# Performance work log

Measured on AMD Instinct MI355X. Metric: run time of the kernel, lower is better.

## Reference

```python
import jax, jax.numpy as jnp
import numpy as np

B, L, F_DIM, H = 4, 384, 640, 128
K_COULOMB = 332.0
DIELECTRIC = 80.0
BN_EPS = 1e-5

# amino-acid charge table, index order 'ACDEFGHIKLMNPQRSTVWY'
_AA = 'ACDEFGHIKLMNPQRSTVWY'
_CHG = {'D': -1.0, 'E': -1.0, 'K': 1.0, 'R': 1.0, 'H': 0.1}
_TABLE = np.zeros((20, 3), dtype=np.float32)
for _i, _aa in enumerate(_AA):
    c = _CHG.get(_aa, 0.0)
    _TABLE[_i, 0 if c > 0 else (1 if c < 0 else 2)] = 1.0
CHG_TABLE = jnp.asarray(_TABLE)


def _conv1d(x, w, b, pad):
    # x: [N, Cin, L], w: [Cout, Cin, K]
    y = jax.lax.conv_general_dilated(x, w, (1,), [(pad, pad)],
                                     dimension_numbers=('NCH', 'OIH', 'NCH'))
    return y + b[None, :, None]


def setup_inputs() -> dict:
    key = jax.random.key(0)
    ks = jax.random.split(key, 32)
    s = 0.05

    def rn(k, shape):
        return (jax.random.normal(k, shape) * s).astype(jnp.float32)

    inp = {
        'features': jax.random.normal(ks[0], (B, L, F_DIM), dtype=jnp.float32),
        'seq_ids': jax.random.randint(ks[1], (B, L), 0, 20, dtype=jnp.int32),
        'structures': (jax.random.normal(ks[2], (B, L, 3)) * 10.0).astype(jnp.float32),
        # charge predictor: Linear(F,H) -> ReLU -> BN(H) -> Linear(H,H//2) -> ReLU -> Linear(H//2,3) -> Softmax
        'W1': rn(ks[3], (F_DIM, H)), 'b1': jnp.zeros((H,), jnp.float32),
        'gamma': jnp.ones((H,), jnp.float32), 'beta': jnp.zeros((H,), jnp.float32),
        'rmean': jnp.zeros((H,), jnp.float32), 'rvar': jnp.ones((H,), jnp.float32),
        'W2': rn(ks[4], (H, H // 2)), 'b2': jnp.zeros((H // 2,), jnp.float32),
        'W3': rn(ks[5], (H // 2, 3)), 'b3': jnp.zeros((3,), jnp.float32),
        # salt bridge detector: Linear(2F+1,H) -> ReLU -> Linear(H,64) -> ReLU -> Linear(64,1) -> Sigmoid
        'sW1': rn(ks[6], (2 * F_DIM + 1, H)), 'sb1': jnp.zeros((H,), jnp.float32),
        'sW2': rn(ks[7], (H, 64)), 'sb2': jnp.zeros((64,), jnp.float32),
        'sW3': rn(ks[8], (64, 1)), 'sb3': jnp.zeros((1,), jnp.float32),
        # potential calculator convs (OIH layout)
        'c1w': rn(ks[9], (16, 1, 5)), 'c1b': jnp.zeros((16,), jnp.float32),
        'c2w': rn(ks[10], (8, 16, 3)), 'c2b': jnp.zeros((8,), jnp.float32),
        'c3w': rn(ks[11], (1, 8, 3)), 'c3b': jnp.zeros((1,), jnp.float32),
    }
    return inp


def reference(features, seq_ids, structures,
              W1, b1, gamma, beta, rmean, rvar, W2, b2, W3, b3,
              sW1, sb1, sW2, sb2, sW3, sb3,
              c1w, c1b, c2w, c2b, c3w, c3b):
    b_, l_, f_ = features.shape

    # true charges from sequence (one-hot pos/neg/neutral)
    true_charges = CHG_TABLE[seq_ids]                               # [B,L,3]

    # --- charge predictor (BatchNorm in eval mode: running stats) ---
    x = features.reshape(-1, f_)
    h = jax.nn.relu(x @ W1 + b1)
    h = gamma * (h - rmean) / jnp.sqrt(rvar + BN_EPS) + beta
    h = jax.nn.relu(h @ W2 + b2)
    pc = jax.nn.softmax(h @ W3 + b3, axis=-1).reshape(b_, l_, 3)    # [B,L,3]

    net_charge = pc[:, :, 0:1] - pc[:, :, 1:2]                      # [B,L,1]

    # --- electrostatic potential: 1D conv stack on [B,1,L] ---
    p = net_charge.transpose(0, 2, 1)                               # [B,1,L]
    p = jax.nn.relu(_conv1d(p, c1w, c1b, 2))
    p = jax.nn.relu(_conv1d(p, c2w, c2b, 1))
    p = _conv1d(p, c3w, c3b, 1)
    potential = p.transpose(0, 2, 1)                                # [B,L,1]

    # --- pairwise distances ---
    diff = structures[:, :, None, :] - structures[:, None, :, :]    # [B,L,L,3]
    D = jnp.sqrt(jnp.sum(diff * diff, axis=-1) + 1e-12)             # [B,L,L]

    # --- salt bridges: vectorized edge-MLP over all (pos i, neg j) pairs ---
    pos = pc[:, :, 0] > pc[:, :, 2]                                 # [B,L]
    neg = pc[:, :, 1] > pc[:, :, 2]                                 # [B,L]
    a, bb, d = sW1[:f_], sW1[f_:2 * f_], sW1[2 * f_]                # split cat([fi,fj,dist]) @ sW1
    fi = features @ a                                               # [B,L,H]
    fj = features @ bb                                              # [B,L,H]
    hid = jax.nn.relu(fi[:, :, None, :] + fj[:, None, :, :] + D[..., None] * d + sb1)  # [B,L,L,H]
    hid2 = jax.nn.relu(hid @ sW2 + sb2)                             # [B,L,L,64]
    prob = jax.nn.sigmoid((hid2 @ sW3 + sb3)[..., 0])               # [B,L,L]
    q = pos[:, :, None] & neg[:, None, :] & (D < 4.0) & (prob > 0.5)
    salt_bridge_masks = (q | q.transpose(0, 2, 1)).astype(jnp.float32)  # [B,L,L]

    # --- Coulomb energy with distance-dependent dielectric ---
    # dielectric = eps * D / 4 -> e_ij = k * q_i q_j / (eps/4 * D^2)
    qc = pc[:, :, 0] - pc[:, :, 1]                                  # [B,L]
    valid = (D < 15.0) & (D > 0.0)
    triu = jnp.triu(jnp.ones((l_, l_), bool), k=1)[None]
    D_safe = jnp.where(valid, D, 1.0)
    e_ij = K_COULOMB * qc[:, :, None] * qc[:, None, :] / ((DIELECTRIC / 4.0) * D_safe * D_safe)
    energy = jnp.sum(jnp.where(valid & triu, e_ij, 0.0), axis=(1, 2))  # [B]

    return (pc, true_charges, net_charge, potential, salt_bridge_masks, energy)
```

## Files before the change

### kernel.cpp

```cpp
#include <hip/hip_runtime.h>

#define LSEQ 384
#define NROWS 1536
#define FDIM 640
#define HDIM 128
#define PART 196608

#define WS_H1P 0
#define WS_FIP (4*PART)
#define WS_FJP (8*PART)
#define WS_FI  (12*PART)
#define WS_FJ  (13*PART)
#define WS_QC  (14*PART)
#define WS_FLAG (WS_QC + NROWS)

#define OUT_PC    0
#define OUT_TC    4608
#define OUT_NET   9216
#define OUT_POT   10752
#define OUT_MASK  12288
#define OUT_EN    602112

__global__ __launch_bounds__(256) void k_gemm(const float* __restrict__ X,
                                              const float* __restrict__ W1,
                                              const float* __restrict__ sW1,
                                              float* __restrict__ ws,
                                              float* __restrict__ out) {
    __shared__ float As[2 * 32 * 34];
    __shared__ float Bs[2 * 32 * 64];
    const int t = threadIdx.x;
    if (blockIdx.x == 0 && blockIdx.y == 0 && blockIdx.z == 0 && t < 4)
        out[OUT_EN + t] = 0.0f;

    const int m0 = blockIdx.x * 32;
    const int gy = blockIdx.y, kz = blockIdx.z;
    const int mat = gy >> 1, half = gy & 1, n0 = half * 64;
    const float* W = (mat == 0) ? W1 : (mat == 1 ? sW1 : sW1 + 640 * 128);
    float* O = ws + (mat == 0 ? WS_H1P : (mat == 1 ? WS_FIP : WS_FJP)) + kz * PART;

    const int a_r = t >> 3, a_c = (t & 7) * 4;
    const int b_r = t >> 4, b_c = (t & 15) * 4;
    const int tx = (t & 15) * 4, ty = (t >> 4) * 2;
    const int k0 = kz * 160;

    float acc[2][4] = {};

    float4 av  = *(const float4*)&X[(m0 + a_r) * FDIM + k0 + a_c];
    float4 bv0 = *(const float4*)&W[(k0 + b_r) * HDIM + n0 + b_c];
    float4 bv1 = *(const float4*)&W[(k0 + b_r + 16) * HDIM + n0 + b_c];
    As[(a_c + 0) * 34 + a_r] = av.x;
    As[(a_c + 1) * 34 + a_r] = av.y;
    As[(a_c + 2) * 34 + a_r] = av.z;
    As[(a_c + 3) * 34 + a_r] = av.w;
    *(float4*)&Bs[b_r * 64 + b_c]        = bv0;
    *(float4*)&Bs[(b_r + 16) * 64 + b_c] = bv1;
    __syncthreads();

    for (int it = 0; it < 5; it++) {
        const int buf = it & 1;
        if (it < 4) {
            const int kk = k0 + (it + 1) * 32;
            av  = *(const float4*)&X[(m0 + a_r) * FDIM + kk + a_c];
            bv0 = *(const float4*)&W[(kk + b_r) * HDIM + n0 + b_c];
            bv1 = *(const float4*)&W[(kk + b_r + 16) * HDIM + n0 + b_c];
        }
        const float* Ab = As + buf * 1088;
        const float* Bb = Bs + buf * 2048;
#pragma unroll
        for (int k = 0; k < 32; k++) {
            float2 a = *(const float2*)&Ab[k * 34 + ty];
            float4 b = *(const float4*)&Bb[k * 64 + tx];
            acc[0][0] = fmaf(a.x, b.x, acc[0][0]);
            acc[0][1] = fmaf(a.x, b.y, acc[0][1]);
            acc[0][2] = fmaf(a.x, b.z, acc[0][2]);
            acc[0][3] = fmaf(a.x, b.w, acc[0][3]);
            acc[1][0] = fmaf(a.y, b.x, acc[1][0]);
            acc[1][1] = fmaf(a.y, b.y, acc[1][1]);
            acc[1][2] = fmaf(a.y, b.z, acc[1][2]);
            acc[1][3] = fmaf(a.y, b.w, acc[1][3]);
        }
        if (it < 4) {
            float* Aw = As + (buf ^ 1) * 1088;
            float* Bw = Bs + (buf ^ 1) * 2048;
            Aw[(a_c + 0) * 34 + a_r] = av.x;
            Aw[(a_c + 1) * 34 + a_r] = av.y;
            Aw[(a_c + 2) * 34 + a_r] = av.z;
            Aw[(a_c + 3) * 34 + a_r] = av.w;
            *(float4*)&Bw[b_r * 64 + b_c]        = bv0;
            *(float4*)&Bw[(b_r + 16) * 64 + b_c] = bv1;
            __syncthreads();
        }
    }
#pragma unroll
    for (int r = 0; r < 2; r++) {
        float4 v = make_float4(acc[r][0], acc[r][1], acc[r][2], acc[r][3]);
        *(float4*)&O[(m0 + ty + r) * HDIM + n0 + tx] = v;
    }
}

__global__ __launch_bounds__(256) void k_row(float* __restrict__ ws,
                                             const float* __restrict__ b1,
                                             const float* __restrict__ gam,
                                             const float* __restrict__ bet,
                                             const float* __restrict__ rmean,
                                             const float* __restrict__ rvar,
                                             const float* __restrict__ W2,
                                             const float* __restrict__ b2,
                                             const float* __restrict__ W3,
                                             const float* __restrict__ b3,
                                             const int* __restrict__ seq,
                                             float* __restrict__ out) {
    const int t = threadIdx.x, w = t >> 6, lane = t & 63;
    const int row = blockIdx.x * 4 + w;
    const long base = (long)row * 128;
    const float* h1p = ws + WS_H1P;
    const float* fip = ws + WS_FIP;
    const float* fjp = ws + WS_FJP;

    {
        float fi0 = fip[base + lane] + fip[PART + base + lane]
                  + fip[2 * PART + base + lane] + fip[3 * PART + base + lane];
        float fi1 = fip[base + 64 + lane] + fip[PART + base + 64 + lane]
                  + fip[2 * PART + base + 64 + lane] + fip[3 * PART + base + 64 + lane];
        float fj0 = fjp[base + lane] + fjp[PART + base + lane]
                  + fjp[2 * PART + base + lane] + fjp[3 * PART + base + lane];
        float fj1 = fjp[base + 64 + lane] + fjp[PART + base + 64 + lane]
                  + fjp[2 * PART + base + 64 + lane] + fjp[3 * PART + base + 64 + lane];
        ws[WS_FI + base + lane]      = fi0;
        ws[WS_FI + base + 64 + lane] = fi1;
        ws[WS_FJ + base + lane]      = fj0;
        ws[WS_FJ + base + 64 + lane] = fj1;
    }

    float h0 = h1p[base + lane] + h1p[PART + base + lane]
             + h1p[2 * PART + base + lane] + h1p[3 * PART + base + lane];
    float h1 = h1p[base + 64 + lane] + h1p[PART + base + 64 + lane]
             + h1p[2 * PART + base + 64 + lane] + h1p[3 * PART + base + 64 + lane];
    h0 = fmaxf(h0 + b1[lane], 0.0f);
    h1 = fmaxf(h1 + b1[64 + lane], 0.0f);
    h0 = gam[lane]      * (h0 - rmean[lane])      / sqrtf(rvar[lane] + 1e-5f)      + bet[lane];
    h1 = gam[64 + lane] * (h1 - rmean[64 + lane]) / sqrtf(rvar[64 + lane] + 1e-5f) + bet[64 + lane];

    float acc = b2[lane];
#pragma unroll
    for (int cc = 0; cc < 64; cc++) {
        float wv0 = W2[cc * 64 + lane];
        float wv1 = W2[(cc + 64) * 64 + lane];
        float hv0 = __uint_as_float(__builtin_amdgcn_readlane(__float_as_uint(h0), cc));
        float hv1 = __uint_as_float(__builtin_amdgcn_readlane(__float_as_uint(h1), cc));
        acc = fmaf(hv0, wv0, acc);
        acc = fmaf(hv1, wv1, acc);
    }
    float h2 = fmaxf(acc, 0.0f);
    float x0 = h2 * W3[lane * 3 + 0];
    float x1 = h2 * W3[lane * 3 + 1];
    float x2 = h2 * W3[lane * 3 + 2];
#pragma unroll
    for (int o = 32; o > 0; o >>= 1) {
        x0 += __shfl_xor(x0, o, 64);
        x1 += __shfl_xor(x1, o, 64);
        x2 += __shfl_xor(x2, o, 64);
    }
    if (lane == 0) {
        float l0 = x0 + b3[0], l1 = x1 + b3[1], l2 = x2 + b3[2];
        float m = fmaxf(l0, fmaxf(l1, l2));
        float e0 = expf(l0 - m), e1 = expf(l1 - m), e2 = expf(l2 - m);
        float s = e0 + e1 + e2;
        float pc0 = e0 / s, pc1 = e1 / s, pc2 = e2 / s;
        out[OUT_PC + row * 3 + 0] = pc0;
        out[OUT_PC + row * 3 + 1] = pc1;
        out[OUT_PC + row * 3 + 2] = pc2;
        float net = pc0 - pc1;
        out[OUT_NET + row] = net;
        ws[WS_QC + row] = net;
        ((int*)(ws + WS_FLAG))[row] = (pc0 > pc2 ? 1 : 0) | (pc1 > pc2 ? 2 : 0);
        int sid = seq[row];
        float c0 = (sid == 6 || sid == 8 || sid == 14) ? 1.0f : 0.0f;
        float c1 = (sid == 2 || sid == 3) ? 1.0f : 0.0f;
        out[OUT_TC + row * 3 + 0] = c0;
        out[OUT_TC + row * 3 + 1] = c1;
        out[OUT_TC + row * 3 + 2] = (c0 == 0.0f && c1 == 0.0f) ? 1.0f : 0.0f;
    }
}

__device__ __forceinline__ float mlp_eval(const float* __restrict__ fi, const float* __restrict__ fj,
                                          int gi, int gj, float D,
                                          float dv0, float dv1, float sb0, float sb1v,
                                          float b2v, float w3l, const float* __restrict__ sW2, int lane) {
    float h0 = fmaxf(fi[(long)gi * 128 + lane]      + fj[(long)gj * 128 + lane]      + D * dv0 + sb0,  0.0f);
    float h1 = fmaxf(fi[(long)gi * 128 + 64 + lane] + fj[(long)gj * 128 + 64 + lane] + D * dv1 + sb1v, 0.0f);
    float a0 = 0.0f, a1 = 0.0f;
#pragma unroll 8
    for (int cc = 0; cc < 64; cc++) {
        float hv0 = __uint_as_float(__builtin_amdgcn_readlane(__float_as_uint(h0), cc));
        float hv1 = __uint_as_float(__builtin_amdgcn_readlane(__float_as_uint(h1), cc));
        a0 = fmaf(hv0, sW2[cc * 64 + lane], a0);
        a1 = fmaf(hv1, sW2[(cc + 64) * 64 + lane], a1);
    }
    float x = fmaxf(a0 + a1 + b2v, 0.0f) * w3l;
#pragma unroll
    for (int o = 32; o > 0; o >>= 1) x += __shfl_xor(x, o, 64);
    return x;
}

__global__ __launch_bounds__(256) void k2(const float* __restrict__ S,
                                          const float* __restrict__ ws,
                                          const float* __restrict__ sW1,
                                          const float* __restrict__ sb1,
                                          const float* __restrict__ sW2,
                                          const float* __restrict__ sb2,
                                          const float* __restrict__ sW3,
                                          const float* __restrict__ sb3,
                                          const float* __restrict__ c1w, const float* __restrict__ c1b,
                                          const float* __restrict__ c2w, const float* __restrict__ c2b,
                                          const float* __restrict__ c3w, const float* __restrict__ c3b,
                                          float* __restrict__ out) {
    __shared__ char smem[6592];
    const int t = threadIdx.x;
    const int bi = blockIdx.x;

    if (bi < 4) {
        float* p0h = (float*)smem;
        const int b = bi;
        for (int idx = t; idx < 392; idx += 256)
            p0h[idx] = (idx >= 4 && idx < 388) ? out[OUT_NET + b * LSEQ + (idx - 4)] : 0.0f;
        __syncthreads();
        for (int pos = t; pos < LSEQ; pos += 256) {
            float p2v[8][3];
#pragma unroll
            for (int o2 = 0; o2 < 8; o2++) {
                float cb = c2b[o2];
#pragma unroll
                for (int d1 = 0; d1 < 3; d1++) p2v[o2][d1] = cb;
            }
            for (int i = 0; i < 16; i++) {
                float p1v[5];
#pragma unroll
                for (int d2 = 0; d2 < 5; d2++) {
                    int q2 = pos - 2 + d2;
                    float a = c1b[i];
#pragma unroll
                    for (int k = 0; k < 5; k++)
                        a = fmaf(p0h[q2 + 2 + k], c1w[i * 5 + k], a);
                    p1v[d2] = (q2 >= 0 && q2 < LSEQ) ? fmaxf(a, 0.0f) : 0.0f;
                }
#pragma unroll
                for (int o2 = 0; o2 < 8; o2++) {
#pragma unroll
                    for (int d1 = 0; d1 < 3; d1++) {
#pragma unroll
                        for (int k = 0; k < 3; k++)
                            p2v[o2][d1] = fmaf(p1v[d1 + k], c2w[(o2 * 16 + i) * 3 + k], p2v[o2][d1]);
                    }
                }
            }
            float acc3 = c3b[0];
#pragma unroll
            for (int o2 = 0; o2 < 8; o2++) {
#pragma unroll
                for (int k = 0; k < 3; k++) {
                    int q1 = pos - 1 + k;
                    float pv = (q1 >= 0 && q1 < LSEQ) ? fmaxf(p2v[o2][k], 0.0f) : 0.0f;
                    acc3 = fmaf(pv, c3w[o2 * 3 + k], acc3);
                }
            }
            out[OUT_POT + b * LSEQ + pos] = acc3;
        }
        return;
    }

    float* sx = (float*)smem;
    float* sy = sx + 384;
    float* sz = sy + 384;
    float* sq = sz + 384;
    unsigned char* sf = (unsigned char*)(sq + 384);
    float* red = (float*)(smem + 6544);

    red = (float*)(smem + 6528);

    const float* qc = ws + WS_QC;
    const int* flags = (const int*)(ws + WS_FLAG);
    const float* fi = ws + WS_FI;
    const float* fj = ws + WS_FJ;

    const int pb = bi - 4;
    const int b = pb / 96;
    const int i0 = (pb % 96) * 4;

    for (int j = t; j < LSEQ; j += 256) {
        int g = b * LSEQ + j;
        sx[j] = S[g * 3 + 0];
        sy[j] = S[g * 3 + 1];
        sz[j] = S[g * 3 + 2];
        sq[j] = qc[g];
        sf[j] = (unsigned char)flags[g];
    }
    __syncthreads();

    const int w = t >> 6, lane = t & 63;
    const int i = i0 + w;
    const int row = b * LSEQ + i;
    const float six = sx[i], siy = sy[i], siz = sz[i], qi = sq[i];
    const int fli = sf[i];
    const bool posi = (fli & 1) != 0, negi = (fli & 2) != 0;
    float* mrow = out + OUT_MASK + (long)row * LSEQ;

    const float* dvec = sW1 + 1280 * 128;
    const float dv0 = dvec[lane], dv1 = dvec[lane + 64];
    const float sb0 = sb1[lane], sb1v = sb1[lane + 64];
    const float w3l = sW3[lane];
    const float b2v = sb2[lane];
    const float b3v = sb3[0];

    float esum = 0.0f;
    for (int j0 = 0; j0 < LSEQ; j0 += 64) {
        const int j = j0 + lane;
        float dx = __fsub_rn(six, sx[j]);
        float dy = __fsub_rn(siy, sy[j]);
        float dz = __fsub_rn(siz, sz[j]);
        float d2 = __fadd_rn(__fadd_rn(__fmul_rn(dx, dx), __fmul_rn(dy, dy)), __fmul_rn(dz, dz));
        d2 = __fadd_rn(d2, 1e-12f);
        float D = __fsqrt_rn(d2);
        if (j > i && D < 15.0f && D > 0.0f) {
            float num = __fmul_rn(__fmul_rn(332.0f, qi), sq[j]);
            float den = __fmul_rn(__fmul_rn(20.0f, D), D);
            esum += __fdiv_rn(num, den);
        }
        int flj = sf[j];
        bool near = (D < 4.0f);
        bool need1 = near && posi && ((flj & 2) != 0);
        bool need2 = near && negi && ((flj & 1) != 0);
        int pk = (need1 ? 1 : 0) | (need2 ? 2 : 0);
        unsigned long long mb = __ballot(pk != 0);
        unsigned long long hitbits = 0ull;
        while (mb) {
            int jl = __ffsll((long long)mb) - 1;
            mb &= mb - 1ull;
            int pf = __shfl(pk, jl, 64);
            float Dj = __shfl(D, jl, 64);
            int gj = b * LSEQ + j0 + jl;
            bool hit = false;
            if (pf & 1) {
                float x = mlp_eval(fi, fj, row, gj, Dj, dv0, dv1, sb0, sb1v, b2v, w3l, sW2, lane);
                hit = (x + b3v) > 0.0f;
            }
            if (!hit && (pf & 2)) {
                float x = mlp_eval(fi, fj, gj, row, Dj, dv0, dv1, sb0, sb1v, b2v, w3l, sW2, lane);
                hit = (x + b3v) > 0.0f;
            }
            if (hit) hitbits |= (1ull << jl);
        }
        mrow[j] = ((hitbits >> lane) & 1ull) ? 1.0f : 0.0f;
    }
#pragma unroll
    for (int o = 32; o > 0; o >>= 1) esum += __shfl_xor(esum, o, 64);
    if (lane == 0) red[w] = esum;
    __syncthreads();
    if (t == 0) {
        float s = red[0] + red[1] + red[2] + red[3];
        atomicAdd(&out[OUT_EN + b], s);
    }
}

extern "C" void kernel_launch(void* const* d_in, const int* in_sizes, int n_in,
                              void* d_out, int out_size, void* d_ws, size_t ws_size,
                              hipStream_t stream) {
    const float* X     = (const float*)d_in[0];
    const int*   seq   = (const int*)d_in[1];
    const float* S     = (const float*)d_in[2];
    const float* W1    = (const float*)d_in[3];
    const float* b1    = (const float*)d_in[4];
    const float* gam   = (const float*)d_in[5];
    const float* bet   = (const float*)d_in[6];
    const float* rmean = (const float*)d_in[7];
    const float* rvar  = (const float*)d_in[8];
    const float* W2    = (const float*)d_in[9];
    const float* b2    = (const float*)d_in[10];
    const float* W3    = (const float*)d_in[11];
    const float* b3    = (const float*)d_in[12];
    const float* sW1   = (const float*)d_in[13];
    const float* sb1   = (const float*)d_in[14];
    const float* sW2   = (const float*)d_in[15];
    const float* sb2   = (const float*)d_in[16];
    const float* sW3   = (const float*)d_in[17];
    const float* sb3   = (const float*)d_in[18];
    const float* c1w   = (const float*)d_in[19];
    const float* c1b   = (const float*)d_in[20];
    const float* c2w   = (const float*)d_in[21];
    const float* c2b   = (const float*)d_in[22];
    const float* c3w   = (const float*)d_in[23];
    const float* c3b   = (const float*)d_in[24];

    float* out = (float*)d_out;
    float* ws  = (float*)d_ws;

    hipLaunchKernelGGL(k_gemm, dim3(48, 6, 4), dim3(256), 0, stream, X, W1, sW1, ws, out);
    hipLaunchKernelGGL(k_row, dim3(384), dim3(256), 0, stream,
                       ws, b1, gam, bet, rmean, rvar, W2, b2, W3, b3, seq, out);
    hipLaunchKernelGGL(k2, dim3(388), dim3(256), 0, stream,
                       S, ws, sW1, sb1, sW2, sb2, sW3, sb3,
                       c1w, c1b, c2w, c2b, c3w, c3b, out);
}
```

Baseline: 165.4 us.

## Fuse charge-predictor GEMM and row MLP into one kernel, drop split-K reduce pass

Merges the GEMM and per-row kernels into a single launch. Blocks 0-95 compute the full-K W1 GEMM for 16 rows, then apply BN and the small MLP and softmax from shared memory. The remaining blocks run the split-K fi/fj GEMM for the salt-bridge weights. The separate pass that summed the split-K partials for fi/fj is removed; mlp_eval now sums the four partials on demand, only for candidate pairs. This saves a launch and a full read/write pass over the workspace, at the cost of a longer serial K loop in the charge blocks and four times as many loads per mlp_eval call.

```diff
diff --git a/kernel.cpp b/kernel.cpp
--- a/kernel.cpp
+++ b/kernel.cpp
@@ -6,12 +6,9 @@
 #define HDIM 128
 #define PART 196608
 
-#define WS_H1P 0
-#define WS_FIP (4*PART)
-#define WS_FJP (8*PART)
-#define WS_FI  (12*PART)
-#define WS_FJ  (13*PART)
-#define WS_QC  (14*PART)
+#define WS_FIP 0
+#define WS_FJP (4*PART)
+#define WS_QC  (8*PART)
 #define WS_FLAG (WS_QC + NROWS)
 
 #define OUT_PC    0
@@ -21,174 +18,249 @@
 #define OUT_MASK  12288
 #define OUT_EN    602112
 
-__global__ __launch_bounds__(256) void k_gemm(const float* __restrict__ X,
-                                              const float* __restrict__ W1,
-                                              const float* __restrict__ sW1,
-                                              float* __restrict__ ws,
-                                              float* __restrict__ out) {
-    __shared__ float As[2 * 32 * 34];
-    __shared__ float Bs[2 * 32 * 64];
+__global__ __launch_bounds__(256) void k1(const float* __restrict__ X,
+                                          const float* __restrict__ W1,
+                                          const float* __restrict__ sW1,
+                                          const float* __restrict__ b1,
+                                          const float* __restrict__ gam,
+                                          const float* __restrict__ bet,
+                                          const float* __restrict__ rmean,
+                                          const float* __restrict__ rvar,
+                                          const float* __restrict__ W2,
+                                          const float* __restrict__ b2,
+                                          const float* __restrict__ W3,
+                                          const float* __restrict__ b3,
+                                          const int* __restrict__ seq,
+                                          float* __restrict__ out,
+                                          float* __restrict__ ws) {
+    __shared__ float smemf[9344];
     const int t = threadIdx.x;
-    if (blockIdx.x == 0 && blockIdx.y == 0 && blockIdx.z == 0 && t < 4)
-        out[OUT_EN + t] = 0.0f;
-
-    const int m0 = blockIdx.x * 32;
-    const int gy = blockIdx.y, kz = blockIdx.z;
-    const int mat = gy >> 1, half = gy & 1, n0 = half * 64;
-    const float* W = (mat == 0) ? W1 : (mat == 1 ? sW1 : sW1 + 640 * 128);
-    float* O = ws + (mat == 0 ? WS_H1P : (mat == 1 ? WS_FIP : WS_FJP)) + kz * PART;
-
-    const int a_r = t >> 3, a_c = (t & 7) * 4;
-    const int b_r = t >> 4, b_c = (t & 15) * 4;
-    const int tx = (t & 15) * 4, ty = (t >> 4) * 2;
-    const int k0 = kz * 160;
-
-    float acc[2][4] = {};
-
-    float4 av  = *(const float4*)&X[(m0 + a_r) * FDIM + k0 + a_c];
-    float4 bv0 = *(const float4*)&W[(k0 + b_r) * HDIM + n0 + b_c];
-    float4 bv1 = *(const float4*)&W[(k0 + b_r + 16) * HDIM + n0 + b_c];
-    As[(a_c + 0) * 34 + a_r] = av.x;
-    As[(a_c + 1) * 34 + a_r] = av.y;
-    As[(a_c + 2) * 34 + a_r] = av.z;
-    As[(a_c + 3) * 34 + a_r] = av.w;
-    *(float4*)&Bs[b_r * 64 + b_c]        = bv0;
-    *(float4*)&Bs[(b_r + 16) * 64 + b_c] = bv1;
-    __syncthreads();
-
-    for (int it = 0; it < 5; it++) {
-        const int buf = it & 1;
-        if (it < 4) {
-            const int kk = k0 + (it + 1) * 32;
-            av  = *(const float4*)&X[(m0 + a_r) * FDIM + kk + a_c];
-            bv0 = *(const float4*)&W[(kk + b_r) * HDIM + n0 + b_c];
-            bv1 = *(const float4*)&W[(kk + b_r + 16) * HDIM + n0 + b_c];
-        }
-        const float* Ab = As + buf * 1088;
-        const float* Bb = Bs + buf * 2048;
-#pragma unroll
-        for (int k = 0; k < 32; k++) {
-            float2 a = *(const float2*)&Ab[k * 34 + ty];
-            float4 b = *(const float4*)&Bb[k * 64 + tx];
-            acc[0][0] = fmaf(a.x, b.x, acc[0][0]);
-            acc[0][1] = fmaf(a.x, b.y, acc[0][1]);
-            acc[0][2] = fmaf(a.x, b.z, acc[0][2]);
-            acc[0][3] = fmaf(a.x, b.w, acc[0][3]);
-            acc[1][0] = fmaf(a.y, b.x, acc[1][0]);
-            acc[1][1] = fmaf(a.y, b.y, acc[1][1]);
-            acc[1][2] = fmaf(a.y, b.z, acc[1][2]);
-            acc[1][3] = fmaf(a.y, b.w, acc[1][3]);
-        }
-        if (it < 4) {
-            float* Aw = As + (buf ^ 1) * 1088;
-            float* Bw = Bs + (buf ^ 1) * 2048;
-            Aw[(a_c + 0) * 34 + a_r] = av.x;
-            Aw[(a_c + 1) * 34 + a_r] = av.y;
-            Aw[(a_c + 2) * 34 + a_r] = av.z;
-            Aw[(a_c + 3) * 34 + a_r] = av.w;
-            *(float4*)&Bw[b_r * 64 + b_c]        = bv0;
-            *(float4*)&Bw[(b_r + 16) * 64 + b_c] = bv1;
-            __syncthreads();
-        }
-    }
-#pragma unroll
-    for (int r = 0; r < 2; r++) {
-        float4 v = make_float4(acc[r][0], acc[r][1], acc[r][2], acc[r][3]);
-        *(float4*)&O[(m0 + ty + r) * HDIM + n0 + tx] = v;
+    const int blk = blockIdx.x;
+
+    if (blk == 0 && t < 4) out[OUT_EN + t] = 0.0f;
+
+    if (blk < 96) {
+        float* As = smemf;
+        float* Bs = smemf + 1152;
+        const int m0 = blk * 16;
+        const int a_r = t >> 4;
+        const int a_c = (t & 15) * 2;
+        const int b_r = t >> 5;
+        const int b_c = (t & 31) * 4;
+        const int tx = (t & 31) * 4;
+        const int ty = (t >> 5) * 2;
+        float acc[2][4] = {};
+
+        float2 av = *(const float2*)&X[(m0 + a_r) * FDIM + a_c];
+        float4 bv0 = *(const float4*)&W1[(b_r) * HDIM + b_c];
+        float4 bv1 = *(const float4*)&W1[(b_r + 8) * HDIM + b_c];
+        float4 bv2 = *(const float4*)&W1[(b_r + 16) * HDIM + b_c];
+        float4 bv3 = *(const float4*)&W1[(b_r + 24) * HDIM + b_c];
+        As[(a_c + 0) * 18 + a_r] = av.x;
+        As[(a_c + 1) * 18 + a_r] = av.y;
+        *(float4*)&Bs[(b_r) * 128 + b_c]      = bv0;
+        *(float4*)&Bs[(b_r + 8) * 128 + b_c]  = bv1;
+        *(float4*)&Bs[(b_r + 16) * 128 + b_c] = bv2;
+        *(float4*)&Bs[(b_r + 24) * 128 + b_c] = bv3;
+        __syncthreads();
+
+        for (int it = 0; it < 20; it++) {
+            const int buf = it & 1;
+            if (it < 19) {
+                const int kk = (it + 1) * 32;
+                av  = *(const float2*)&X[(m0 + a_r) * FDIM + kk + a_c];
+                bv0 = *(const float4*)&W1[(kk + b_r) * HDIM + b_c];
+                bv1 = *(const float4*)&W1[(kk + b_r + 8) * HDIM + b_c];
+                bv2 = *(const float4*)&W1[(kk + b_r + 16) * HDIM + b_c];
+                bv3 = *(const float4*)&W1[(kk + b_r + 24) * HDIM + b_c];
+            }
+            const float* Ab = As + buf * 576;
+            const float* Bb = Bs + buf * 4096;
+#pragma unroll
+            for (int k = 0; k < 32; k++) {
+                float2 a = *(const float2*)&Ab[k * 18 + ty];
+                float4 b = *(const float4*)&Bb[k * 128 + tx];
+                acc[0][0] = fmaf(a.x, b.x, acc[0][0]);
+                acc[0][1] = fmaf(a.x, b.y, acc[0][1]);
+                acc[0][2] = fmaf(a.x, b.z, acc[0][2]);
+                acc[0][3] = fmaf(a.x, b.w, acc[0][3]);
+                acc[1][0] = fmaf(a.y, b.x, acc[1][0]);
+                acc[1][1] = fmaf(a.y, b.y, acc[1][1]);
+                acc[1][2] = fmaf(a.y, b.z, acc[1][2]);
+                acc[1][3] = fmaf(a.y, b.w, acc[1][3]);
+            }
+            if (it < 19) {
+                float* Aw = As + (buf ^ 1) * 576;
+                float* Bw = Bs + (buf ^ 1) * 4096;
+                Aw[(a_c + 0) * 18 + a_r] = av.x;
+                Aw[(a_c + 1) * 18 + a_r] = av.y;
+                *(float4*)&Bw[(b_r) * 128 + b_c]      = bv0;
+                *(float4*)&Bw[(b_r + 8) * 128 + b_c]  = bv1;
+                *(float4*)&Bw[(b_r + 16) * 128 + b_c] = bv2;
+                *(float4*)&Bw[(b_r + 24) * 128 + b_c] = bv3;
+                __syncthreads();
+            }
+        }
+        __syncthreads();
+
+        float* hs = smemf;
+        {
+            float4 b1v = *(const float4*)&b1[tx];
+            float4 g4  = *(const float4*)&gam[tx];
+            float4 be4 = *(const float4*)&bet[tx];
+            float4 rm4 = *(const float4*)&rmean[tx];
+            float4 rv4 = *(const float4*)&rvar[tx];
+            float rs0 = 1.0f / sqrtf(rv4.x + 1e-5f);
+            float rs1 = 1.0f / sqrtf(rv4.y + 1e-5f);
+            float rs2 = 1.0f / sqrtf(rv4.z + 1e-5f);
+            float rs3 = 1.0f / sqrtf(rv4.w + 1e-5f);
+#pragma unroll
+            for (int r = 0; r < 2; r++) {
+                float v0 = g4.x * (fmaxf(acc[r][0] + b1v.x, 0.0f) - rm4.x) * rs0 + be4.x;
+                float v1 = g4.y * (fmaxf(acc[r][1] + b1v.y, 0.0f) - rm4.y) * rs1 + be4.y;
+                float v2 = g4.z * (fmaxf(acc[r][2] + b1v.z, 0.0f) - rm4.z) * rs2 + be4.z;
+                float v3 = g4.w * (fmaxf(acc[r][3] + b1v.w, 0.0f) - rm4.w) * rs3 + be4.w;
+                *(float4*)&hs[(ty + r) * 132 + tx] = make_float4(v0, v1, v2, v3);
+            }
+        }
+        __syncthreads();
+
+        const int w = t >> 6, lane = t & 63;
+        float h0r[4], h1r[4], acc2[4];
+#pragma unroll
+        for (int r = 0; r < 4; r++) {
+            h0r[r] = hs[(w * 4 + r) * 132 + lane];
+            h1r[r] = hs[(w * 4 + r) * 132 + 64 + lane];
+            acc2[r] = b2[lane];
+        }
+#pragma unroll
+        for (int cc = 0; cc < 64; cc++) {
+            float wv0 = W2[cc * 64 + lane];
+            float wv1 = W2[(cc + 64) * 64 + lane];
+#pragma unroll
+            for (int r = 0; r < 4; r++) {
+                float hv0 = __uint_as_float(__builtin_amdgcn_readlane(__float_as_uint(h0r[r]), cc));
+                float hv1 = __uint_as_float(__builtin_amdgcn_readlane(__float_as_uint(h1r[r]), cc));
+                acc2[r] = fmaf(hv0, wv0, acc2[r]);
+                acc2[r] = fmaf(hv1, wv1, acc2[r]);
+            }
+        }
+        float w30 = W3[lane * 3 + 0], w31 = W3[lane * 3 + 1], w32 = W3[lane * 3 + 2];
+#pragma unroll
+        for (int r = 0; r < 4; r++) {
+            float h2 = fmaxf(acc2[r], 0.0f);
+            float x0 = h2 * w30, x1 = h2 * w31, x2 = h2 * w32;
+#pragma unroll
+            for (int o = 32; o > 0; o >>= 1) {
+                x0 += __shfl_xor(x0, o, 64);
+                x1 += __shfl_xor(x1, o, 64);
+                x2 += __shfl_xor(x2, o, 64);
+            }
+            if (lane == 0) {
+                int row = m0 + w * 4 + r;
+                float l0 = x0 + b3[0], l1 = x1 + b3[1], l2 = x2 + b3[2];
+                float m = fmaxf(l0, fmaxf(l1, l2));
+                float e0 = expf(l0 - m), e1 = expf(l1 - m), e2 = expf(l2 - m);
+                float s = e0 + e1 + e2;
+                float pc0 = e0 / s, pc1 = e1 / s, pc2 = e2 / s;
+                out[OUT_PC + row * 3 + 0] = pc0;
+                out[OUT_PC + row * 3 + 1] = pc1;
+                out[OUT_PC + row * 3 + 2] = pc2;
+                float net = pc0 - pc1;
+                out[OUT_NET + row] = net;
+                ws[WS_QC + row] = net;
+                ((int*)(ws + WS_FLAG))[row] = (pc0 > pc2 ? 1 : 0) | (pc1 > pc2 ? 2 : 0);
+                int sid = seq[row];
+                float c0 = (sid == 6 || sid == 8 || sid == 14) ? 1.0f : 0.0f;
+                float c1 = (sid == 2 || sid == 3) ? 1.0f : 0.0f;
+                out[OUT_TC + row * 3 + 0] = c0;
+                out[OUT_TC + row * 3 + 1] = c1;
+                out[OUT_TC + row * 3 + 2] = (c0 == 0.0f && c1 == 0.0f) ? 1.0f : 0.0f;
+            }
+        }
+    } else {
+        float* As = smemf;
+        float* Bs = smemf + 2176;
+        const int bi = blk - 96;
+        const int mt = bi >> 4, rem = bi & 15;
+        const int mat = rem >> 3, half = (rem >> 2) & 1, kz = rem & 3;
+        const int m0 = mt * 32, n0 = half * 64;
+        const float* W = sW1 + mat * 640 * 128;
+        float* O = ws + (mat == 0 ? WS_FIP : WS_FJP) + kz * PART;
+
+        const int a_r = t >> 3, a_c = (t & 7) * 4;
+        const int b_r = t >> 4, b_c = (t & 15) * 4;
+        const int tx = (t & 15) * 4, ty = (t >> 4) * 2;
+        const int k0 = kz * 160;
+
+        float acc[2][4] = {};
+
+        float4 av  = *(const float4*)&X[(m0 + a_r) * FDIM + k0 + a_c];
+        float4 bv0 = *(const float4*)&W[(k0 + b_r) * HDIM + n0 + b_c];
+        float4 bv1 = *(const float4*)&W[(k0 + b_r + 16) * HDIM + n0 + b_c];
+        As[(a_c + 0) * 34 + a_r] = av.x;
+        As[(a_c + 1) * 34 + a_r] = av.y;
+        As[(a_c + 2) * 34 + a_r] = av.z;
+        As[(a_c + 3) * 34 + a_r] = av.w;
+        *(float4*)&Bs[b_r * 64 + b_c]        = bv0;
+        *(float4*)&Bs[(b_r + 16) * 64 + b_c] = bv1;
+        __syncthreads();
+
+        for (int it = 0; it < 5; it++) {
+            const int buf = it & 1;
+            if (it < 4) {
+                const int kk = k0 + (it + 1) * 32;
+                av  = *(const float4*)&X[(m0 + a_r) * FDIM + kk + a_c];
+                bv0 = *(const float4*)&W[(kk + b_r) * HDIM + n0 + b_c];
+                bv1 = *(const float4*)&W[(kk + b_r + 16) * HDIM + n0 + b_c];
+            }
+            const float* Ab = As + buf * 1088;
+            const float* Bb = Bs + buf * 2048;
+#pragma unroll
+            for (int k = 0; k < 32; k++) {
+                float2 a = *(const float2*)&Ab[k * 34 + ty];
+                float4 b = *(const float4*)&Bb[k * 64 + tx];
+                acc[0][0] = fmaf(a.x, b.x, acc[0][0]);
+                acc[0][1] = fmaf(a.x, b.y, acc[0][1]);
+                acc[0][2] = fmaf(a.x, b.z, acc[0][2]);
+                acc[0][3] = fmaf(a.x, b.w, acc[0][3]);
+                acc[1][0] = fmaf(a.y, b.x, acc[1][0]);
+                acc[1][1] = fmaf(a.y, b.y, acc[1][1]);
+                acc[1][2] = fmaf(a.y, b.z, acc[1][2]);
+                acc[1][3] = fmaf(a.y, b.w, acc[1][3]);
+            }
+            if (it < 4) {
+                float* Aw = As + (buf ^ 1) * 1088;
+                float* Bw = Bs + (buf ^ 1) * 2048;
+                Aw[(a_c + 0) * 34 + a_r] = av.x;
+                Aw[(a_c + 1) * 34 + a_r] = av.y;
+                Aw[(a_c + 2) * 34 + a_r] = av.z;
+                Aw[(a_c + 3) * 34 + a_r] = av.w;
+                *(float4*)&Bw[b_r * 64 + b_c]        = bv0;
+                *(float4*)&Bw[(b_r + 16) * 64 + b_c] = bv1;
+                __syncthreads();
+            }
+        }
+#pragma unroll
+        for (int r = 0; r < 2; r++) {
+            float4 v = make_float4(acc[r][0], acc[r][1], acc[r][2], acc[r][3]);
+            *(float4*)&O[(m0 + ty + r) * HDIM + n0 + tx] = v;
+        }
     }
 }
 
-__global__ __launch_bounds__(256) void k_row(float* __restrict__ ws,
-                                             const float* __restrict__ b1,
-                                             const float* __restrict__ gam,
-                                             const float* __restrict__ bet,
-                                             const float* __restrict__ rmean,
-                                             const float* __restrict__ rvar,
-                                             const float* __restrict__ W2,
-                                             const float* __restrict__ b2,
-                                             const float* __restrict__ W3,
-                                             const float* __restrict__ b3,
-                                             const int* __restrict__ seq,
-                                             float* __restrict__ out) {
-    const int t = threadIdx.x, w = t >> 6, lane = t & 63;
-    const int row = blockIdx.x * 4 + w;
-    const long base = (long)row * 128;
-    const float* h1p = ws + WS_H1P;
-    const float* fip = ws + WS_FIP;
-    const float* fjp = ws + WS_FJP;
-
-    {
-        float fi0 = fip[base + lane] + fip[PART + base + lane]
-                  + fip[2 * PART + base + lane] + fip[3 * PART + base + lane];
-        float fi1 = fip[base + 64 + lane] + fip[PART + base + 64 + lane]
-                  + fip[2 * PART + base + 64 + lane] + fip[3 * PART + base + 64 + lane];
-        float fj0 = fjp[base + lane] + fjp[PART + base + lane]
-                  + fjp[2 * PART + base + lane] + fjp[3 * PART + base + lane];
-        float fj1 = fjp[base + 64 + lane] + fjp[PART + base + 64 + lane]
-                  + fjp[2 * PART + base + 64 + lane] + fjp[3 * PART + base + 64 + lane];
-        ws[WS_FI + base + lane]      = fi0;
-        ws[WS_FI + base + 64 + lane] = fi1;
-        ws[WS_FJ + base + lane]      = fj0;
-        ws[WS_FJ + base + 64 + lane] = fj1;
-    }
-
-    float h0 = h1p[base + lane] + h1p[PART + base + lane]
-             + h1p[2 * PART + base + lane] + h1p[3 * PART + base + lane];
-    float h1 = h1p[base + 64 + lane] + h1p[PART + base + 64 + lane]
-             + h1p[2 * PART + base + 64 + lane] + h1p[3 * PART + base + 64 + lane];
-    h0 = fmaxf(h0 + b1[lane], 0.0f);
-    h1 = fmaxf(h1 + b1[64 + lane], 0.0f);
-    h0 = gam[lane]      * (h0 - rmean[lane])      / sqrtf(rvar[lane] + 1e-5f)      + bet[lane];
-    h1 = gam[64 + lane] * (h1 - rmean[64 + lane]) / sqrtf(rvar[64 + lane] + 1e-5f) + bet[64 + lane];
-
-    float acc = b2[lane];
-#pragma unroll
-    for (int cc = 0; cc < 64; cc++) {
-        float wv0 = W2[cc * 64 + lane];
-        float wv1 = W2[(cc + 64) * 64 + lane];
-        float hv0 = __uint_as_float(__builtin_amdgcn_readlane(__float_as_uint(h0), cc));
-        float hv1 = __uint_as_float(__builtin_amdgcn_readlane(__float_as_uint(h1), cc));
-        acc = fmaf(hv0, wv0, acc);
-        acc = fmaf(hv1, wv1, acc);
-    }
-    float h2 = fmaxf(acc, 0.0f);
-    float x0 = h2 * W3[lane * 3 + 0];
-    float x1 = h2 * W3[lane * 3 + 1];
-    float x2 = h2 * W3[lane * 3 + 2];
-#pragma unroll
-    for (int o = 32; o > 0; o >>= 1) {
-        x0 += __shfl_xor(x0, o, 64);
-        x1 += __shfl_xor(x1, o, 64);
-        x2 += __shfl_xor(x2, o, 64);
-    }
-    if (lane == 0) {
-        float l0 = x0 + b3[0], l1 = x1 + b3[1], l2 = x2 + b3[2];
-        float m = fmaxf(l0, fmaxf(l1, l2));
-        float e0 = expf(l0 - m), e1 = expf(l1 - m), e2 = expf(l2 - m);
-        float s = e0 + e1 + e2;
-        float pc0 = e0 / s, pc1 = e1 / s, pc2 = e2 / s;
-        out[OUT_PC + row * 3 + 0] = pc0;
-        out[OUT_PC + row * 3 + 1] = pc1;
-        out[OUT_PC + row * 3 + 2] = pc2;
-        float net = pc0 - pc1;
-        out[OUT_NET + row] = net;
-        ws[WS_QC + row] = net;
-        ((int*)(ws + WS_FLAG))[row] = (pc0 > pc2 ? 1 : 0) | (pc1 > pc2 ? 2 : 0);
-        int sid = seq[row];
-        float c0 = (sid == 6 || sid == 8 || sid == 14) ? 1.0f : 0.0f;
-        float c1 = (sid == 2 || sid == 3) ? 1.0f : 0.0f;
-        out[OUT_TC + row * 3 + 0] = c0;
-        out[OUT_TC + row * 3 + 1] = c1;
-        out[OUT_TC + row * 3 + 2] = (c0 == 0.0f && c1 == 0.0f) ? 1.0f : 0.0f;
-    }
-}
-
-__device__ __forceinline__ float mlp_eval(const float* __restrict__ fi, const float* __restrict__ fj,
+__device__ __forceinline__ float mlp_eval(const float* __restrict__ fiP, const float* __restrict__ fjP,
                                           int gi, int gj, float D,
                                           float dv0, float dv1, float sb0, float sb1v,
                                           float b2v, float w3l, const float* __restrict__ sW2, int lane) {
-    float h0 = fmaxf(fi[(long)gi * 128 + lane]      + fj[(long)gj * 128 + lane]      + D * dv0 + sb0,  0.0f);
-    float h1 = fmaxf(fi[(long)gi * 128 + 64 + lane] + fj[(long)gj * 128 + 64 + lane] + D * dv1 + sb1v, 0.0f);
+    const long bi0 = (long)gi * 128 + lane;
+    const long bj0 = (long)gj * 128 + lane;
+    float fi0 = fiP[bi0]      + fiP[PART + bi0]      + fiP[2 * PART + bi0]      + fiP[3 * PART + bi0];
+    float fi1 = fiP[bi0 + 64] + fiP[PART + bi0 + 64] + fiP[2 * PART + bi0 + 64] + fiP[3 * PART + bi0 + 64];
+    float fj0 = fjP[bj0]      + fjP[PART + bj0]      + fjP[2 * PART + bj0]      + fjP[3 * PART + bj0];
+    float fj1 = fjP[bj0 + 64] + fjP[PART + bj0 + 64] + fjP[2 * PART + bj0 + 64] + fjP[3 * PART + bj0 + 64];
+    float h0 = fmaxf(fi0 + fj0 + D * dv0 + sb0,  0.0f);
+    float h1 = fmaxf(fi1 + fj1 + D * dv1 + sb1v, 0.0f);
     float a0 = 0.0f, a1 = 0.0f;
 #pragma unroll 8
     for (int cc = 0; cc < 64; cc++) {
@@ -274,14 +346,12 @@
     float* sz = sy + 384;
     float* sq = sz + 384;
     unsigned char* sf = (unsigned char*)(sq + 384);
-    float* red = (float*)(smem + 6544);
-
-    red = (float*)(smem + 6528);
+    float* red = (float*)(smem + 6528);
 
     const float* qc = ws + WS_QC;
     const int* flags = (const int*)(ws + WS_FLAG);
-    const float* fi = ws + WS_FI;
-    const float* fj = ws + WS_FJ;
+    const float* fiP = ws + WS_FIP;
+    const float* fjP = ws + WS_FJP;
 
     const int pb = bi - 4;
     const int b = pb / 96;
@@ -341,11 +411,11 @@
             int gj = b * LSEQ + j0 + jl;
             bool hit = false;
             if (pf & 1) {
-                float x = mlp_eval(fi, fj, row, gj, Dj, dv0, dv1, sb0, sb1v, b2v, w3l, sW2, lane);
+                float x = mlp_eval(fiP, fjP, row, gj, Dj, dv0, dv1, sb0, sb1v, b2v, w3l, sW2, lane);
                 hit = (x + b3v) > 0.0f;
             }
             if (!hit && (pf & 2)) {
-                float x = mlp_eval(fi, fj, gj, row, Dj, dv0, dv1, sb0, sb1v, b2v, w3l, sW2, lane);
+                float x = mlp_eval(fiP, fjP, gj, row, Dj, dv0, dv1, sb0, sb1v, b2v, w3l, sW2, lane);
                 hit = (x + b3v) > 0.0f;
             }
             if (hit) hitbits |= (1ull << jl);
@@ -394,9 +464,9 @@
     float* out = (float*)d_out;
     float* ws  = (float*)d_ws;
 
-    hipLaunchKernelGGL(k_gemm, dim3(48, 6, 4), dim3(256), 0, stream, X, W1, sW1, ws, out);
-    hipLaunchKernelGGL(k_row, dim3(384), dim3(256), 0, stream,
-                       ws, b1, gam, bet, rmean, rvar, W2, b2, W3, b3, seq, out);
+    hipLaunchKernelGGL(k1, dim3(864), dim3(256), 0, stream,
+                       X, W1, sW1, b1, gam, bet, rmean, rvar, W2, b2, W3, b3,
+                       seq, out, ws);
     hipLaunchKernelGGL(k2, dim3(388), dim3(256), 0, stream,
                        S, ws, sW1, sb1, sW2, sb2, sW3, sb3,
                        c1w, c1b, c2w, c2b, c3w, c3b, out);
```

New measurement: 171.9 us. 1.04x slower.
